# Optimization experiments

Measured on AMD Instinct MI355X. Metric: run time of the kernel, lower is better.

The kernel has to match this reference:

```python
import jax, jax.numpy as jnp
import numpy as np


def setup_inputs() -> dict:
    key = jax.random.key(0)
    k1, k2 = jax.random.split(key)
    inp = jax.random.normal(k1, (32, 3, 224, 224), dtype=jnp.float32)
    kernels_theta = jax.random.normal(k2, (64, 5, 5), dtype=jnp.float32)
    return {"inp": inp, "kernels_theta": kernels_theta}


def reference(inp, kernels_theta):
    # Faithful to original: the per-channel loop overwrites actual_tensor,
    # so only the LAST input channel contributes to the output.
    x = inp[:, -1:, :, :]  # [B, 1, H, W]
    # Each output channel correlates the same single-channel 2D kernel.
    w = kernels_theta[:, None, :, :]  # [OC, 1, k, k]
    out = jax.lax.conv_general_dilated(
        x, w,
        window_strides=(1, 1),
        padding='VALID',
        dimension_numbers=('NCHW', 'OIHW', 'NCHW'),
    )  # [B, OC, o, o] cross-correlation (matches elementwise-mul+sum)
    # output[i] = actual_tensor.transpose(0, 2) swaps the two spatial axes.
    return jnp.swapaxes(out, 2, 3)
```

## Files before the change

kernel.cpp:

```cpp
#include <hip/hip_runtime.h>


#define IMG    224
#define OHW    220
#define FLAT   (OHW * OHW)
#define NOUT   64
#define KW     5
#define BLOCK  256
#define QPB    (BLOCK * 4)
#define NBX    48
#define OG     8
#define COLS   10
#define PR     228
#define SLAB   (COLS * PR)

typedef float floatx4 __attribute__((ext_vector_type(4)));

__global__ __launch_bounds__(BLOCK, 4)
void ConvolutionalLayer_88742614270062_kernel(const float* __restrict__ inp,
                                              const float* __restrict__ kt,
                                              float* __restrict__ out) {
    __shared__ float s[SLAB];

    const int n   = blockIdx.z;
    const int og  = blockIdx.y * OG;
    const int f0  = blockIdx.x * QPB;
    const int jlo = f0 / OHW;

    const float* __restrict__ xb = inp + ((size_t)(n * 3 + 2)) * (IMG * IMG);

    for (int idx = threadIdx.x; idx < IMG * COLS; idx += BLOCK) {
        int r   = idx / COLS;
        int c   = idx - r * COLS;
        int col = jlo + c;
        s[c * PR + r] = (col < IMG) ? xb[r * IMG + col] : 0.0f;
    }
    __syncthreads();

    const int  f    = f0 + (int)threadIdx.x * 4;
    const bool live = (f < FLAT);
    const int  fc   = live ? f : (FLAT - 4);
    const int  j    = fc / OHW;
    const int  i4   = fc - j * OHW;
    const int  cj   = j - jlo;

    float w8[KW][8];
#pragma unroll
    for (int b = 0; b < KW; ++b) {
        const floatx4* p = reinterpret_cast<const floatx4*>(&s[(cj + b) * PR + i4]);
        floatx4 lo = p[0];
        floatx4 hi = p[1];
        w8[b][0] = lo.x; w8[b][1] = lo.y; w8[b][2] = lo.z; w8[b][3] = lo.w;
        w8[b][4] = hi.x; w8[b][5] = hi.y; w8[b][6] = hi.z; w8[b][7] = hi.w;
    }

    const float* __restrict__ wk = kt + og * (KW * KW);
    float* __restrict__ op = out + ((size_t)(n * NOUT + og)) * FLAT + f;

#pragma unroll
    for (int oc = 0; oc < OG; ++oc) {
        float a0 = 0.f, a1 = 0.f, a2 = 0.f, a3 = 0.f;
#pragma unroll
        for (int a = 0; a < KW; ++a) {
#pragma unroll
            for (int b = 0; b < KW; ++b) {
                float w = wk[oc * (KW * KW) + a * KW + b];
                a0 = fmaf(w, w8[b][a    ], a0);
                a1 = fmaf(w, w8[b][a + 1], a1);
                a2 = fmaf(w, w8[b][a + 2], a2);
                a3 = fmaf(w, w8[b][a + 3], a3);
            }
        }
        if (live) {
            floatx4 v = { a0, a1, a2, a3 };
            __builtin_nontemporal_store(v,
                reinterpret_cast<floatx4*>(op + (size_t)oc * FLAT));
        }
    }
}

extern "C" void kernel_launch(void* const* d_in, const int* in_sizes, int n_in,
                              void* d_out, int out_size, void* d_ws, size_t ws_size,
                              hipStream_t stream) {
    const float* inp = (const float*)d_in[0];
    const float* kt  = (const float*)d_in[1];
    float* out       = (float*)d_out;

    dim3 grid(NBX, NOUT / OG, 32);
    ConvolutionalLayer_88742614270062_kernel<<<grid, BLOCK, 0, stream>>>(inp, kt, out);
}
```

Before: 85.81 us.

## Assign one output channel per block and loop over larger spatial tiles

```diff
diff --git a/kernel.cpp b/kernel.cpp
--- a/kernel.cpp
+++ b/kernel.cpp
@@ -7,10 +7,10 @@
 #define NOUT   64
 #define KW     5
 #define BLOCK  256
-#define QPB    (BLOCK * 4)
-#define NBX    48
-#define OG     8
-#define COLS   10
+#define QPT    8
+#define OPB    (BLOCK * 4 * QPT)
+#define NBX    6
+#define COLS   43
 #define PR     228
 #define SLAB   (COLS * PR)
 
@@ -23,8 +23,8 @@
     __shared__ float s[SLAB];
 
     const int n   = blockIdx.z;
-    const int og  = blockIdx.y * OG;
-    const int f0  = blockIdx.x * QPB;
+    const int o   = blockIdx.y;
+    const int f0  = blockIdx.x * OPB;
     const int jlo = f0 / OHW;
 
     const float* __restrict__ xb = inp + ((size_t)(n * 3 + 2)) * (IMG * IMG);
@@ -37,44 +37,50 @@
     }
     __syncthreads();
 
-    const int  f    = f0 + (int)threadIdx.x * 4;
-    const bool live = (f < FLAT);
-    const int  fc   = live ? f : (FLAT - 4);
-    const int  j    = fc / OHW;
-    const int  i4   = fc - j * OHW;
-    const int  cj   = j - jlo;
+    const float* __restrict__ wk = kt + o * (KW * KW);
+    float w[KW * KW];
+#pragma unroll
+    for (int t = 0; t < KW * KW; ++t) w[t] = wk[t];
 
-    float w8[KW][8];
+    float* __restrict__ plane = out + ((size_t)(n * NOUT + o)) * FLAT;
+
+#pragma unroll 2
+    for (int it = 0; it < QPT; ++it) {
+        const int  f    = f0 + (it << 10) + ((int)threadIdx.x << 2);
+        const bool live = (f < FLAT);
+        const int  fc   = live ? f : (FLAT - 4);
+        const int  j    = fc / OHW;
+        const int  i4   = fc - j * OHW;
+        const int  cj   = j - jlo;
+
+        float w8[KW][8];
 #pragma unroll
-    for (int b = 0; b < KW; ++b) {
-        const floatx4* p = reinterpret_cast<const floatx4*>(&s[(cj + b) * PR + i4]);
-        floatx4 lo = p[0];
-        floatx4 hi = p[1];
-        w8[b][0] = lo.x; w8[b][1] = lo.y; w8[b][2] = lo.z; w8[b][3] = lo.w;
-        w8[b][4] = hi.x; w8[b][5] = hi.y; w8[b][6] = hi.z; w8[b][7] = hi.w;
-    }
+        for (int b = 0; b < KW; ++b) {
+            const floatx4* p =
+                reinterpret_cast<const floatx4*>(&s[(cj + b) * PR + i4]);
+            floatx4 lo = p[0];
+            floatx4 hi = p[1];
+            w8[b][0] = lo.x; w8[b][1] = lo.y; w8[b][2] = lo.z; w8[b][3] = lo.w;
+            w8[b][4] = hi.x; w8[b][5] = hi.y; w8[b][6] = hi.z; w8[b][7] = hi.w;
+        }
 
-    const float* __restrict__ wk = kt + og * (KW * KW);
-    float* __restrict__ op = out + ((size_t)(n * NOUT + og)) * FLAT + f;
-
-#pragma unroll
-    for (int oc = 0; oc < OG; ++oc) {
         float a0 = 0.f, a1 = 0.f, a2 = 0.f, a3 = 0.f;
 #pragma unroll
         for (int a = 0; a < KW; ++a) {
 #pragma unroll
             for (int b = 0; b < KW; ++b) {
-                float w = wk[oc * (KW * KW) + a * KW + b];
-                a0 = fmaf(w, w8[b][a    ], a0);
-                a1 = fmaf(w, w8[b][a + 1], a1);
-                a2 = fmaf(w, w8[b][a + 2], a2);
-                a3 = fmaf(w, w8[b][a + 3], a3);
+                float ww = w[a * KW + b];
+                a0 = fmaf(ww, w8[b][a    ], a0);
+                a1 = fmaf(ww, w8[b][a + 1], a1);
+                a2 = fmaf(ww, w8[b][a + 2], a2);
+                a3 = fmaf(ww, w8[b][a + 3], a3);
             }
         }
+
         if (live) {
             floatx4 v = { a0, a1, a2, a3 };
             __builtin_nontemporal_store(v,
-                reinterpret_cast<floatx4*>(op + (size_t)oc * FLAT));
+                reinterpret_cast<floatx4*>(plane + f));
         }
     }
 }
@@ -86,6 +92,6 @@
     const float* kt  = (const float*)d_in[1];
     float* out       = (float*)d_out;
 
-    dim3 grid(NBX, NOUT / OG, 32);
+    dim3 grid(NBX, NOUT, 32);
     ConvolutionalLayer_88742614270062_kernel<<<grid, BLOCK, 0, stream>>>(inp, kt, out);
 }
```

New measurement: 193.7 us. +125.7%, slower.
